# Performance work log

Measured on AMD Instinct MI355X. Metric: run time of the kernel, lower is better.

## Reference

```python
import jax, jax.numpy as jnp
import numpy as np
import math

H = 128  # hidden_dim
RADIUS = 30.0


def _lin(x, w, b):
    return x @ w + b


def _masked_softmax(logits, mask):
    return jax.nn.softmax(jnp.where(mask, logits, -1e9), axis=-1)


def setup_inputs() -> dict:
    key = jax.random.key(0)
    ks = iter(jax.random.split(key, 64))

    def p(shape, s=0.02):
        return (jax.random.normal(next(ks), shape, jnp.float32) * s)

    B, N, T, M, L = 2, 48, 24, 192, 20
    inp = {
        'agents_state': jax.random.normal(next(ks), (B, N, T, 5), jnp.float32),
        'agents_mask': jnp.ones((B, N, T), jnp.float32),
        'map_polylines': jax.random.normal(next(ks), (B, M, L, 2), jnp.float32),
        'map_poly_mask': jnp.ones((B, M), jnp.float32),
        'map_poly_type': jax.random.randint(next(ks), (B, M), 0, 4),
        'map_tl_status': jax.random.randint(next(ks), (B, M), 0, 8),
        'map_on_route': jax.random.randint(next(ks), (B, M), 0, 2),
        # AgentStateEncoder
        'ae_w0': p((5, H)), 'ae_b0': p((H,)), 'ae_w1': p((H, H)), 'ae_b1': p((H,)),
        'ae_w2': p((H, H)), 'ae_b2': p((H,)),
        # MapPolylineNodeEncoder point_mlp
        'mp_w0': p((2, H)), 'mp_b0': p((H,)), 'mp_w1': p((H, H)), 'mp_b1': p((H,)),
        'type_emb': p((4, H)), 'tl_emb': p((8, H)), 'route_emb': p((2, H)),
        'mo_w0': p((H, H)), 'mo_b0': p((H,)), 'mo_w1': p((H, H)), 'mo_b1': p((H,)),
        # map_rel_mlp (3 -> H -> 1)
        'mr_w0': p((3, H)), 'mr_b0': p((H,)), 'mr_w1': p((H, 1)), 'mr_b1': p((1,)),
        # nbr_rel_mlp (5 -> H -> 1)
        'nr_w0': p((5, H)), 'nr_b0': p((H,)), 'nr_w1': p((H, 1)), 'nr_b1': p((1,)),
        # tau_out (3H -> H -> 64)
        'to_w0': p((3 * H, H)), 'to_b0': p((H,)), 'to_w1': p((H, 64)), 'to_b1': p((64,)),
    }
    return inp


def reference(agents_state, agents_mask, map_polylines, map_poly_mask,
              map_poly_type, map_tl_status, map_on_route,
              ae_w0, ae_b0, ae_w1, ae_b1, ae_w2, ae_b2,
              mp_w0, mp_b0, mp_w1, mp_b1, type_emb, tl_emb, route_emb,
              mo_w0, mo_b0, mo_w1, mo_b1,
              mr_w0, mr_b0, mr_w1, mr_b1,
              nr_w0, nr_b0, nr_w1, nr_b1,
              to_w0, to_b0, to_w1, to_b1):
    B, N, T, _ = agents_state.shape
    a_mask = agents_mask > 0.5
    a_feat = agents_state[..., :5]

    # --- MapPolylineNodeEncoder ---
    m = map_poly_mask > 0.5
    h = jax.nn.relu(_lin(jax.nn.relu(_lin(map_polylines, mp_w0, mp_b0)), mp_w1, mp_b1))  # B,M,L,H
    h = h.max(axis=2)  # B,M,H
    pt = jnp.clip(map_poly_type, 0, type_emb.shape[0] - 1)
    tl = jnp.clip(map_tl_status, 0, tl_emb.shape[0] - 1)
    rt = jnp.clip(map_on_route, 0, route_emb.shape[0] - 1)
    h = h + type_emb[pt] + tl_emb[tl] + route_emb[rt]
    h = _lin(jax.nn.relu(_lin(h, mo_w0, mo_b0)), mo_w1, mo_b1)
    map_node = h * m[..., None].astype(h.dtype)  # B,M,D
    map_center = map_polylines.mean(axis=2)  # B,M,2

    # --- AgentStateEncoder ---
    a = jax.nn.relu(_lin(a_feat, ae_w0, ae_b0))
    a = jax.nn.relu(_lin(a, ae_w1, ae_b1))
    a_emb = _lin(a, ae_w2, ae_b2) * a_mask[..., None].astype(a.dtype)  # B,N,T,D

    # --- map cross-attention with relative-position bias ---
    agent_pos = a_feat[..., 0:2]
    rel = map_center[:, None, None, :, :] - agent_pos[:, :, :, None, :]  # B,N,T,M,2
    dist = jnp.linalg.norm(rel, axis=-1, keepdims=True)
    rel_feat = jnp.concatenate([rel, dist], axis=-1)  # B,N,T,M,3
    rel_score = _lin(jax.nn.relu(_lin(rel_feat, mr_w0, mr_b0)), mr_w1, mr_b1)[..., 0]  # B,N,T,M
    dot = jnp.einsum('bntd,bmd->bntm', a_emb, map_node) / math.sqrt(map_node.shape[-1])
    attn = _masked_softmax(dot + rel_score, m[:, None, None, :])
    map_ctx = jnp.einsum('bntm,bmd->bntd', attn, map_node)

    # --- neighbor graph attention ---
    pos = a_feat[..., 0:2]
    vel = a_feat[..., 3:5]
    rel_pos = jnp.transpose(pos[:, :, None] - pos[:, None, :], (0, 1, 3, 2, 4))  # B,N,T,N,2
    rel_vel = jnp.transpose(vel[:, :, None] - vel[:, None, :], (0, 1, 3, 2, 4))
    dist_ij = jnp.linalg.norm(rel_pos, axis=-1, keepdims=True)  # B,N,T,N,1
    rel_ij = jnp.concatenate([rel_pos, rel_vel, dist_ij], axis=-1)  # B,N,T,N,5
    nbr_score = _lin(jax.nn.relu(_lin(rel_ij, nr_w0, nr_b0)), nr_w1, nr_b1)[..., 0]  # B,N,T,N

    valid_i = a_mask[..., None]  # B,N,T,1
    valid_j = jnp.transpose(a_mask, (0, 2, 1))[:, None, :, :]  # B,1,T,N
    radius_ok = dist_ij[..., 0] <= RADIUS
    not_self = ~jnp.eye(N, dtype=bool)[None, :, None, :]  # 1,N,1,N
    nbr_mask = valid_i & valid_j & radius_ok & not_self

    dot_n = jnp.einsum('bntd,bjtd->bntj', a_emb, a_emb) / math.sqrt(a_emb.shape[-1])
    w_n = _masked_softmax(dot_n + nbr_score, nbr_mask)  # B,N,T,N
    nbr_ctx = jnp.einsum('bntj,bjtd->bntd', w_n, a_emb)

    tau = jnp.concatenate([a_emb, map_ctx, nbr_ctx], axis=-1)
    tau = _lin(jax.nn.relu(_lin(tau, to_w0, to_b0)), to_w1, to_b1)
    tau = tau * a_mask[..., None].astype(tau.dtype)
    return tau, map_ctx, nbr_ctx
```

## Files before the change

kernel.cpp:

```cpp
#include <hip/hip_runtime.h>
#include <math.h>

#define HH 128
#define BB 2
#define NN 48
#define TT 24
#define MM 192
#define LL 20
#define NT (BB*NN*TT)
#define RSQRT_H 0.08838834764831845f
#define RADIUS_C 30.0f

struct P {
    const float *astate, *amask, *polylines, *poly_mask;
    const int *ptype, *tlst, *route;
    const float *ae_w0,*ae_b0,*ae_w1,*ae_b1,*ae_w2,*ae_b2;
    const float *mp_w0,*mp_b0,*mp_w1,*mp_b1;
    const float *type_emb,*tl_emb,*route_emb;
    const float *mo_w0,*mo_b0,*mo_w1,*mo_b1;
    const float *mr_w0,*mr_b0,*mr_w1,*mr_b1;
    const float *nr_w0,*nr_b0,*nr_w1,*nr_b1;
    const float *to_w0,*to_b0,*to_w1,*to_b1;
    float *tau,*map_ctx,*nbr_ctx;
    float *a_emb,*map_node,*map_nodeT,*map_center;
};

struct SME { float pts[LL*2]; float h1T[HH][LL]; float mx[2][HH]; float hb[HH]; float pr[2][HH]; float hb2[HH]; };
struct SAG { float xin[2][5]; float h1[2][HH]; float h2[2][HH]; float p1[2][2][HH]; };

struct SF {
    float4 aq4L[HH];
    float  mctx[4][HH];
    float  nctx[4][HH];
    float  pc[2][4][HH];
    union {
        struct {
            float4 w4L[HH];
            float  w1L[HH];
            float  lg[4][MM];
            float4 p4L[MM];
            float  invL[4];
        } m;
        struct {
            float  pjL[NN][8];
            float4 wAL[HH];
            float4 wBL[HH];
            float  sPL[4][4][NN];
            float  dPL[4][4][NN];
            float  lgN[4][NN];
            float4 pN[NN];
        } n;
        struct {
            float4 xinT[3*HH];
            float4 h1T[HH];
        } t;
    } u;
};

__device__ void do_map_enc(const P& p, SME& s, int bm) {
    int tid = threadIdx.x, pp = tid >> 7, c = tid & 127;
    if (tid < LL*2) s.pts[tid] = p.polylines[(size_t)bm*LL*2 + tid];
    __syncthreads();
    {
        float w0x = p.mp_w0[c], w0y = p.mp_w0[HH + c], b0 = p.mp_b0[c];
        #pragma unroll
        for (int i = 0; i < 10; ++i) {
            int pt_ = pp*10 + i;
            s.h1T[c][pt_] = fmaxf(fmaf(s.pts[2*pt_], w0x, fmaf(s.pts[2*pt_+1], w0y, b0)), 0.f);
        }
    }
    if (tid < 2) {
        float sum = 0.f;
        for (int q = 0; q < LL; ++q) sum += s.pts[2*q + tid];
        p.map_center[bm*2 + tid] = sum * (1.0f / LL);
    }
    __syncthreads();
    {
        float acc[10];
        float b1 = p.mp_b1[c];
        #pragma unroll
        for (int i = 0; i < 10; ++i) acc[i] = b1;
        for (int k = 0; k < HH; ++k) {
            float wv = p.mp_w1[k*HH + c];
            const float* hrow = &s.h1T[k][pp*10];
            #pragma unroll
            for (int i = 0; i < 10; ++i) acc[i] = fmaf(hrow[i], wv, acc[i]);
        }
        float m10 = acc[0];
        #pragma unroll
        for (int i = 1; i < 10; ++i) m10 = fmaxf(m10, acc[i]);
        s.mx[pp][c] = m10;
    }
    __syncthreads();
    if (tid < HH) {
        float hm = fmaxf(fmaxf(s.mx[0][c], s.mx[1][c]), 0.f);
        int pt = p.ptype[bm]; pt = pt < 0 ? 0 : (pt > 3 ? 3 : pt);
        int tv = p.tlst[bm];  tv = tv < 0 ? 0 : (tv > 7 ? 7 : tv);
        int rv = p.route[bm]; rv = rv < 0 ? 0 : (rv > 1 ? 1 : rv);
        hm += p.type_emb[pt*HH + c] + p.tl_emb[tv*HH + c] + p.route_emb[rv*HH + c];
        s.hb[c] = hm;
    }
    __syncthreads();
    {
        float sum = 0.f;
        int k0 = pp*64;
        for (int k = k0; k < k0 + 64; ++k) sum = fmaf(s.hb[k], p.mo_w0[k*HH + c], sum);
        s.pr[pp][c] = sum;
    }
    __syncthreads();
    if (tid < HH) s.hb2[c] = fmaxf(s.pr[0][c] + s.pr[1][c] + p.mo_b0[c], 0.f);
    __syncthreads();
    {
        float sum = 0.f;
        int k0 = pp*64;
        for (int k = k0; k < k0 + 64; ++k) sum = fmaf(s.hb2[k], p.mo_w1[k*HH + c], sum);
        s.pr[pp][c] = sum;
    }
    __syncthreads();
    if (tid < HH) {
        float a3 = s.pr[0][c] + s.pr[1][c] + p.mo_b1[c];
        float mk = (p.poly_mask[bm] > 0.5f) ? 1.f : 0.f;
        float v = a3 * mk;
        p.map_node[(size_t)bm*HH + c] = v;
        int b = bm / MM, m = bm % MM;
        p.map_nodeT[((size_t)b*HH + c)*MM + m] = v;
    }
}

__device__ void do_agent_enc(const P& p, SAG& s, int r0) {
    int tid = threadIdx.x, h = tid >> 7, c = tid & 127;
    if (tid < 10) s.xin[tid/5][tid%5] = p.astate[(size_t)r0*5 + tid];
    __syncthreads();
    if (h == 0) {
        float b = p.ae_b0[c];
        float w[5];
        #pragma unroll
        for (int i = 0; i < 5; ++i) w[i] = p.ae_w0[i*HH + c];
        #pragma unroll
        for (int r = 0; r < 2; ++r) {
            float v = b;
            #pragma unroll
            for (int i = 0; i < 5; ++i) v = fmaf(s.xin[r][i], w[i], v);
            s.h1[r][c] = fmaxf(v, 0.f);
        }
    }
    __syncthreads();
    {
        float a0 = 0.f, a1 = 0.f;
        int k0 = h*64;
        for (int k = k0; k < k0 + 64; ++k) {
            float wv = p.ae_w1[k*HH + c];
            a0 = fmaf(s.h1[0][k], wv, a0);
            a1 = fmaf(s.h1[1][k], wv, a1);
        }
        s.p1[h][0][c] = a0; s.p1[h][1][c] = a1;
    }
    __syncthreads();
    {
        int r = h;
        s.h2[r][c] = fmaxf(s.p1[0][r][c] + s.p1[1][r][c] + p.ae_b1[c], 0.f);
    }
    __syncthreads();
    {
        float a0 = 0.f, a1 = 0.f;
        int k0 = h*64;
        for (int k = k0; k < k0 + 64; ++k) {
            float wv = p.ae_w2[k*HH + c];
            a0 = fmaf(s.h2[0][k], wv, a0);
            a1 = fmaf(s.h2[1][k], wv, a1);
        }
        s.p1[h][0][c] = a0; s.p1[h][1][c] = a1;
    }
    __syncthreads();
    {
        int r = h;
        int row = r0 + r;
        p.a_emb[(size_t)row*HH + c] = (s.p1[0][r][c] + s.p1[1][r][c] + p.ae_b2[c]) * p.amask[row];
    }
}

__global__ __launch_bounds__(256) void k_enc(P p) {
    __shared__ __align__(16) char smraw[(sizeof(SME) > sizeof(SAG)) ? sizeof(SME) : sizeof(SAG)];
    int task = blockIdx.x;
    if (task < BB*MM) do_map_enc(p, *(SME*)smraw, task);
    else              do_agent_enc(p, *(SAG*)smraw, (task - BB*MM)*2);
}

__global__ __launch_bounds__(256) void k_fat(P p) {
    __shared__ __align__(16) SF s;
    int task = blockIdx.x;
    int b    = task / (TT*12);
    int rem  = task % (TT*12);
    int t    = rem / 12;
    int n0   = (rem % 12) * 4;
    int tid  = threadIdx.x;

    int row0 = (b*NN + n0)*TT + t;

    for (int idx = tid; idx < 4*HH; idx += 256) {
        int r = idx >> 7, k = idx & 127;
        ((float*)&s.aq4L[k])[r] = p.a_emb[(size_t)(row0 + r*TT)*HH + k];
    }
    if (tid < HH) {
        int k = tid;
        s.u.m.w4L[k] = make_float4(p.mr_w0[k], p.mr_w0[HH+k], p.mr_w0[2*HH+k], p.mr_b0[k]);
        s.u.m.w1L[k] = p.mr_w1[k];
    }

    float rx[4], ry[4], rd[4];
    if (tid < MM) {
        float mcx = p.map_center[(b*MM + tid)*2];
        float mcy = p.map_center[(b*MM + tid)*2 + 1];
        #pragma unroll
        for (int r = 0; r < 4; ++r) {
            float px = p.astate[(size_t)(row0 + r*TT)*5];
            float py = p.astate[(size_t)(row0 + r*TT)*5 + 1];
            rx[r] = mcx - px; ry[r] = mcy - py;
            rd[r] = sqrtf(rx[r]*rx[r] + ry[r]*ry[r]);
        }
    }
    __syncthreads();

    if (tid < MM) {
        const float* mnc = p.map_nodeT + (size_t)b*HH*MM + tid;
        float sacc[4] = {0.f,0.f,0.f,0.f};
        float dt4[4]  = {0.f,0.f,0.f,0.f};
        const float4* w1q4 = (const float4*)s.u.m.w1L;
        for (int kq = 0; kq < HH/4; ++kq) {
            float4 w1q = w1q4[kq];
            #pragma unroll
            for (int j = 0; j < 4; ++j) {
                int k = kq*4 + j;
                float4 w  = s.u.m.w4L[k];
                float4 aq = s.aq4L[k];
                float  w1 = ((const float*)&w1q)[j];
                float  mn = mnc[(size_t)k*MM];
                #pragma unroll
                for (int r = 0; r < 4; ++r) {
                    float hv = fmaf(rx[r], w.x, fmaf(ry[r], w.y, fmaf(rd[r], w.z, w.w)));
                    sacc[r] = fmaf(fmaxf(hv, 0.f), w1, sacc[r]);
                }
                dt4[0] = fmaf(aq.x, mn, dt4[0]);
                dt4[1] = fmaf(aq.y, mn, dt4[1]);
                dt4[2] = fmaf(aq.z, mn, dt4[2]);
                dt4[3] = fmaf(aq.w, mn, dt4[3]);
            }
        }
        float pm = p.poly_mask[b*MM + tid];
        float b1 = p.mr_b1[0];
        #pragma unroll
        for (int r = 0; r < 4; ++r) {
            float lgt = fmaf(dt4[r], RSQRT_H, sacc[r] + b1);
            s.u.m.lg[r][tid] = (pm > 0.5f) ? lgt : -1e9f;
        }
    }
    __syncthreads();

    {
        int r = tid >> 6, l = tid & 63;
        float v = fmaxf(fmaxf(s.u.m.lg[r][l], s.u.m.lg[r][l+64]), s.u.m.lg[r][l+128]);
        #pragma unroll
        for (int o = 32; o > 0; o >>= 1) v = fmaxf(v, __shfl_xor(v, o));
        float e0 = expf(s.u.m.lg[r][l] - v);
        float e1 = expf(s.u.m.lg[r][l+64] - v);
        float e2 = expf(s.u.m.lg[r][l+128] - v);
        s.u.m.lg[r][l] = e0; s.u.m.lg[r][l+64] = e1; s.u.m.lg[r][l+128] = e2;
        float sm = e0 + e1 + e2;
        #pragma unroll
        for (int o = 32; o > 0; o >>= 1) sm += __shfl_xor(sm, o);
        if (l == 0) s.u.m.invL[r] = 1.0f / sm;
    }
    __syncthreads();
    if (tid < MM) {
        s.u.m.p4L[tid] = make_float4(s.u.m.lg[0][tid]*s.u.m.invL[0], s.u.m.lg[1][tid]*s.u.m.invL[1],
                                     s.u.m.lg[2][tid]*s.u.m.invL[2], s.u.m.lg[3][tid]*s.u.m.invL[3]);
    }
    __syncthreads();

    {
        int half = tid >> 7, c = tid & 127;
        float a0=0.f, a1=0.f, a2=0.f, a3=0.f;
        const float* mnb = p.map_node + ((size_t)b*MM + half*96)*HH + c;
        for (int m = 0; m < 96; ++m) {
            float mv = mnb[(size_t)m*HH];
            float4 pp4 = s.u.m.p4L[half*96 + m];
            a0 = fmaf(pp4.x, mv, a0); a1 = fmaf(pp4.y, mv, a1);
            a2 = fmaf(pp4.z, mv, a2); a3 = fmaf(pp4.w, mv, a3);
        }
        s.pc[half][0][c]=a0; s.pc[half][1][c]=a1; s.pc[half][2][c]=a2; s.pc[half][3][c]=a3;
    }
    __syncthreads();
    for (int idx = tid; idx < 4*HH; idx += 256) {
        int r = idx >> 7, c = idx & 127;
        float v = s.pc[0][r][c] + s.pc[1][r][c];
        s.mctx[r][c] = v;
        p.map_ctx[(size_t)(row0 + r*TT)*HH + c] = v;
    }
    __syncthreads();

    if (tid < NN) {
        int rj = (b*NN + tid)*TT + t;
        s.u.n.pjL[tid][0] = p.astate[(size_t)rj*5];
        s.u.n.pjL[tid][1] = p.astate[(size_t)rj*5 + 1];
        s.u.n.pjL[tid][2] = p.astate[(size_t)rj*5 + 3];
        s.u.n.pjL[tid][3] = p.astate[(size_t)rj*5 + 4];
        s.u.n.pjL[tid][4] = p.amask[rj];
    }
    if (tid < HH) {
        int k = tid;
        s.u.n.wAL[k] = make_float4(p.nr_w0[k], p.nr_w0[HH+k], p.nr_w0[2*HH+k], p.nr_w0[3*HH+k]);
        s.u.n.wBL[k] = make_float4(p.nr_w0[4*HH+k], p.nr_b0[k], p.nr_w1[k], 0.f);
    }
    __syncthreads();

    {
        int j  = tid % 48;
        int kg = tid / 48;
        if (kg < 4) {
            float jx = s.u.n.pjL[j][0], jy = s.u.n.pjL[j][1];
            float jvx = s.u.n.pjL[j][2], jvy = s.u.n.pjL[j][3];
            float dx[4], dy[4], dvx[4], dvy[4], dd[4];
            #pragma unroll
            for (int r = 0; r < 4; ++r) {
                int ni = n0 + r;
                dx[r]  = s.u.n.pjL[ni][0] - jx;  dy[r]  = s.u.n.pjL[ni][1] - jy;
                dvx[r] = s.u.n.pjL[ni][2] - jvx; dvy[r] = s.u.n.pjL[ni][3] - jvy;
                dd[r]  = sqrtf(dx[r]*dx[r] + dy[r]*dy[r]);
            }
            const float* aj = p.a_emb + ((size_t)(b*NN + j)*TT + t)*HH;
            float sr[4]  = {0.f,0.f,0.f,0.f};
            float dtn[4] = {0.f,0.f,0.f,0.f};
            int k0 = kg*32;
            #pragma unroll 4
            for (int kk = 0; kk < 32; ++kk) {
                int k = k0 + kk;
                float4 wa = s.u.n.wAL[k], wb = s.u.n.wBL[k];
                float4 aq = s.aq4L[k];
                float  av = aj[k];
                #pragma unroll
                for (int r = 0; r < 4; ++r) {
                    float hv = fmaf(dx[r], wa.x, fmaf(dy[r], wa.y,
                               fmaf(dvx[r], wa.z, fmaf(dvy[r], wa.w,
                               fmaf(dd[r], wb.x, wb.y)))));
                    sr[r] = fmaf(fmaxf(hv, 0.f), wb.z, sr[r]);
                }
                dtn[0] = fmaf(aq.x, av, dtn[0]); dtn[1] = fmaf(aq.y, av, dtn[1]);
                dtn[2] = fmaf(aq.z, av, dtn[2]); dtn[3] = fmaf(aq.w, av, dtn[3]);
            }
            #pragma unroll
            for (int r = 0; r < 4; ++r) { s.u.n.sPL[kg][r][j] = sr[r]; s.u.n.dPL[kg][r][j] = dtn[r]; }
        }
    }
    __syncthreads();

    {
        float b1 = p.nr_b1[0];
        for (int idx = tid; idx < 4*NN; idx += 256) {
            int r = idx / NN, jj = idx % NN;
            int ni = n0 + r;
            float ss  = s.u.n.sPL[0][r][jj] + s.u.n.sPL[1][r][jj] + s.u.n.sPL[2][r][jj] + s.u.n.sPL[3][r][jj] + b1;
            float do2 = s.u.n.dPL[0][r][jj] + s.u.n.dPL[1][r][jj] + s.u.n.dPL[2][r][jj] + s.u.n.dPL[3][r][jj];
            float ddx = s.u.n.pjL[ni][0] - s.u.n.pjL[jj][0];
            float ddy = s.u.n.pjL[ni][1] - s.u.n.pjL[jj][1];
            float dist = sqrtf(ddx*ddx + ddy*ddy);
            bool ok = (s.u.n.pjL[ni][4] > 0.5f) && (s.u.n.pjL[jj][4] > 0.5f) &&
                      (dist <= RADIUS_C) && (jj != ni);
            s.u.n.lgN[r][jj] = ok ? fmaf(do2, RSQRT_H, ss) : -1e9f;
        }
    }
    __syncthreads();

    {
        int r = tid >> 6, l = tid & 63;
        float v = (l < NN) ? s.u.n.lgN[r][l] : -3.4e38f;
        #pragma unroll
        for (int o = 32; o > 0; o >>= 1) v = fmaxf(v, __shfl_xor(v, o));
        float e = (l < NN) ? expf(s.u.n.lgN[r][l] - v) : 0.f;
        float sm = e;
        #pragma unroll
        for (int o = 32; o > 0; o >>= 1) sm += __shfl_xor(sm, o);
        if (l < NN) s.u.n.lgN[r][l] = e / sm;
    }
    __syncthreads();
    if (tid < NN) {
        s.u.n.pN[tid] = make_float4(s.u.n.lgN[0][tid], s.u.n.lgN[1][tid],
                                    s.u.n.lgN[2][tid], s.u.n.lgN[3][tid]);
    }
    __syncthreads();

    {
        int half = tid >> 7, c = tid & 127;
        float a0=0.f, a1=0.f, a2=0.f, a3=0.f;
        for (int jj = half*24; jj < half*24 + 24; ++jj) {
            float av = p.a_emb[((size_t)(b*NN + jj)*TT + t)*HH + c];
            float4 pp4 = s.u.n.pN[jj];
            a0 = fmaf(pp4.x, av, a0); a1 = fmaf(pp4.y, av, a1);
            a2 = fmaf(pp4.z, av, a2); a3 = fmaf(pp4.w, av, a3);
        }
        s.pc[half][0][c]=a0; s.pc[half][1][c]=a1; s.pc[half][2][c]=a2; s.pc[half][3][c]=a3;
    }
    __syncthreads();
    for (int idx = tid; idx < 4*HH; idx += 256) {
        int r = idx >> 7, c = idx & 127;
        float v = s.pc[0][r][c] + s.pc[1][r][c];
        s.nctx[r][c] = v;
        p.nbr_ctx[(size_t)(row0 + r*TT)*HH + c] = v;
    }
    __syncthreads();

    for (int idx = tid; idx < 3*HH; idx += 256) {
        if (idx < HH) {
            s.u.t.xinT[idx] = s.aq4L[idx];
        } else if (idx < 2*HH) {
            int k = idx - HH;
            s.u.t.xinT[idx] = make_float4(s.mctx[0][k], s.mctx[1][k], s.mctx[2][k], s.mctx[3][k]);
        } else {
            int k = idx - 2*HH;
            s.u.t.xinT[idx] = make_float4(s.nctx[0][k], s.nctx[1][k], s.nctx[2][k], s.nctx[3][k]);
        }
    }
    __syncthreads();
    {
        int c = tid & 127, h = tid >> 7;
        float acc[4] = {0,0,0,0};
        for (int k = h*192; k < h*192 + 192; ++k) {
            float wv = p.to_w0[k*HH + c];
            float4 x4 = s.u.t.xinT[k];
            acc[0]=fmaf(x4.x,wv,acc[0]); acc[1]=fmaf(x4.y,wv,acc[1]);
            acc[2]=fmaf(x4.z,wv,acc[2]); acc[3]=fmaf(x4.w,wv,acc[3]);
        }
        #pragma unroll
        for (int r = 0; r < 4; ++r) s.pc[h][r][c] = acc[r];
    }
    __syncthreads();
    for (int idx = tid; idx < 4*HH; idx += 256) {
        int r = idx >> 7, k = idx & 127;
        ((float*)&s.u.t.h1T[k])[r] = fmaxf(s.pc[0][r][k] + s.pc[1][r][k] + p.to_b0[k], 0.f);
    }
    __syncthreads();
    {
        int kh = tid >> 7, rc = tid & 127;
        int r = rc >> 6, c2 = rc & 63;
        float acc = 0.f;
        for (int k = kh*64; k < kh*64 + 64; ++k)
            acc = fmaf(((const float*)&s.u.t.h1T[k])[r], p.to_w1[k*64 + c2], acc);
        s.pc[kh][r][c2] = acc;
    }
    __syncthreads();
    if (tid < 128) {
        int r = tid >> 6, c2 = tid & 63;
        int row = row0 + r*TT;
        float v = (s.pc[0][r][c2] + s.pc[1][r][c2] + p.to_b1[c2]) * p.amask[row];
        p.tau[(size_t)row*64 + c2] = v;
    }
    __syncthreads();
    if (tid < 128) {
        int r = 2 + (tid >> 6), c2 = tid & 63;
        int row = row0 + r*TT;
        float acc = 0.f;
        for (int k = 0; k < HH; ++k)
            acc = fmaf(((const float*)&s.u.t.h1T[k])[r], p.to_w1[k*64 + c2], acc);
        float v = (acc + p.to_b1[c2]) * p.amask[row];
        p.tau[(size_t)row*64 + c2] = v;
    }
}

extern "C" void kernel_launch(void* const* d_in, const int* in_sizes, int n_in,
                              void* d_out, int out_size, void* d_ws, size_t ws_size,
                              hipStream_t stream)
{
    P p;
    p.astate    = (const float*)d_in[0];
    p.amask     = (const float*)d_in[1];
    p.polylines = (const float*)d_in[2];
    p.poly_mask = (const float*)d_in[3];
    p.ptype     = (const int*)d_in[4];
    p.tlst      = (const int*)d_in[5];
    p.route     = (const int*)d_in[6];
    p.ae_w0 = (const float*)d_in[7];  p.ae_b0 = (const float*)d_in[8];
    p.ae_w1 = (const float*)d_in[9];  p.ae_b1 = (const float*)d_in[10];
    p.ae_w2 = (const float*)d_in[11]; p.ae_b2 = (const float*)d_in[12];
    p.mp_w0 = (const float*)d_in[13]; p.mp_b0 = (const float*)d_in[14];
    p.mp_w1 = (const float*)d_in[15]; p.mp_b1 = (const float*)d_in[16];
    p.type_emb  = (const float*)d_in[17];
    p.tl_emb    = (const float*)d_in[18];
    p.route_emb = (const float*)d_in[19];
    p.mo_w0 = (const float*)d_in[20]; p.mo_b0 = (const float*)d_in[21];
    p.mo_w1 = (const float*)d_in[22]; p.mo_b1 = (const float*)d_in[23];
    p.mr_w0 = (const float*)d_in[24]; p.mr_b0 = (const float*)d_in[25];
    p.mr_w1 = (const float*)d_in[26]; p.mr_b1 = (const float*)d_in[27];
    p.nr_w0 = (const float*)d_in[28]; p.nr_b0 = (const float*)d_in[29];
    p.nr_w1 = (const float*)d_in[30]; p.nr_b1 = (const float*)d_in[31];
    p.to_w0 = (const float*)d_in[32]; p.to_b0 = (const float*)d_in[33];
    p.to_w1 = (const float*)d_in[34]; p.to_b1 = (const float*)d_in[35];

    p.tau     = (float*)d_out;
    p.map_ctx = (float*)d_out + (size_t)NT*64;
    p.nbr_ctx = p.map_ctx + (size_t)NT*HH;

    float* ws    = (float*)d_ws;
    p.a_emb      = ws;
    p.map_node   = p.a_emb + (size_t)NT*HH;
    p.map_nodeT  = p.map_node + (size_t)BB*MM*HH;
    p.map_center = p.map_nodeT + (size_t)BB*MM*HH;

    k_enc<<<BB*MM + NT/2, 256, 0, stream>>>(p);
    k_fat<<<BB*TT*12,     256, 0, stream>>>(p);
}
```

Baseline: 184.2 us.

## Double k_fat block size and split reductions across more thread groups

Raises k_fat to 512 threads and splits each reduction stage (map logits, map context, neighbor scores, neighbor context, both tau MLP layers) into more partial-sum groups, then combines them through shared memory. This adds parallelism within each of the 576 blocks, so per-thread serial loops get shorter and latency is easier to hide. It also changes the map encoder's h1 shared layout from transposed to row-major, which alters the LDS access pattern. In exchange it uses more shared memory and adds partial-sum buffers, which may lower occupancy.

```diff
diff --git a/kernel.cpp b/kernel.cpp
--- a/kernel.cpp
+++ b/kernel.cpp
@@ -25,18 +25,20 @@
     float *a_emb,*map_node,*map_nodeT,*map_center;
 };
 
-struct SME { float pts[LL*2]; float h1T[HH][LL]; float mx[2][HH]; float hb[HH]; float pr[2][HH]; float hb2[HH]; };
+struct SME { float pts[LL*2]; float h1[LL][HH]; float mx[2][HH]; float hb[HH]; float pr[2][HH]; float hb2[HH]; };
 struct SAG { float xin[2][5]; float h1[2][HH]; float h2[2][HH]; float p1[2][2][HH]; };
 
 struct SF {
     float4 aq4L[HH];
     float  mctx[4][HH];
     float  nctx[4][HH];
-    float  pc[2][4][HH];
+    float  pc[4][4][HH];
     union {
         struct {
             float4 w4L[HH];
             float  w1L[HH];
+            float4 pS[2][MM];
+            float4 pD[2][MM];
             float  lg[4][MM];
             float4 p4L[MM];
             float  invL[4];
@@ -45,8 +47,8 @@
             float  pjL[NN][8];
             float4 wAL[HH];
             float4 wBL[HH];
-            float  sPL[4][4][NN];
-            float  dPL[4][4][NN];
+            float  sPL[8][4][NN];
+            float  dPL[8][4][NN];
             float  lgN[4][NN];
             float4 pN[NN];
         } n;
@@ -65,8 +67,8 @@
         float w0x = p.mp_w0[c], w0y = p.mp_w0[HH + c], b0 = p.mp_b0[c];
         #pragma unroll
         for (int i = 0; i < 10; ++i) {
-            int pt_ = pp*10 + i;
-            s.h1T[c][pt_] = fmaxf(fmaf(s.pts[2*pt_], w0x, fmaf(s.pts[2*pt_+1], w0y, b0)), 0.f);
+            int pt_ = pp + 2*i;
+            s.h1[pt_][c] = fmaxf(fmaf(s.pts[2*pt_], w0x, fmaf(s.pts[2*pt_+1], w0y, b0)), 0.f);
         }
     }
     if (tid < 2) {
@@ -82,9 +84,8 @@
         for (int i = 0; i < 10; ++i) acc[i] = b1;
         for (int k = 0; k < HH; ++k) {
             float wv = p.mp_w1[k*HH + c];
-            const float* hrow = &s.h1T[k][pp*10];
             #pragma unroll
-            for (int i = 0; i < 10; ++i) acc[i] = fmaf(hrow[i], wv, acc[i]);
+            for (int i = 0; i < 10; ++i) acc[i] = fmaf(s.h1[pp + 2*i][k], wv, acc[i]);
         }
         float m10 = acc[0];
         #pragma unroll
@@ -186,7 +187,7 @@
     else              do_agent_enc(p, *(SAG*)smraw, (task - BB*MM)*2);
 }
 
-__global__ __launch_bounds__(256) void k_fat(P p) {
+__global__ __launch_bounds__(512) void k_fat(P p) {
     __shared__ __align__(16) SF s;
     int task = blockIdx.x;
     int b    = task / (TT*12);
@@ -197,8 +198,8 @@
 
     int row0 = (b*NN + n0)*TT + t;
 
-    for (int idx = tid; idx < 4*HH; idx += 256) {
-        int r = idx >> 7, k = idx & 127;
+    {
+        int r = tid >> 7, k = tid & 127;
         ((float*)&s.aq4L[k])[r] = p.a_emb[(size_t)(row0 + r*TT)*HH + k];
     }
     if (tid < HH) {
@@ -207,10 +208,12 @@
         s.u.m.w1L[k] = p.mr_w1[k];
     }
 
+    int g  = tid >> 8;
+    int ml = tid & 255;
     float rx[4], ry[4], rd[4];
-    if (tid < MM) {
-        float mcx = p.map_center[(b*MM + tid)*2];
-        float mcy = p.map_center[(b*MM + tid)*2 + 1];
+    if (ml < MM) {
+        float mcx = p.map_center[(b*MM + ml)*2];
+        float mcy = p.map_center[(b*MM + ml)*2 + 1];
         #pragma unroll
         for (int r = 0; r < 4; ++r) {
             float px = p.astate[(size_t)(row0 + r*TT)*5];
@@ -221,42 +224,50 @@
     }
     __syncthreads();
 
-    if (tid < MM) {
-        const float* mnc = p.map_nodeT + (size_t)b*HH*MM + tid;
+    if (ml < MM) {
+        const float* mnc = p.map_nodeT + (size_t)b*HH*MM + ml;
         float sacc[4] = {0.f,0.f,0.f,0.f};
         float dt4[4]  = {0.f,0.f,0.f,0.f};
-        const float4* w1q4 = (const float4*)s.u.m.w1L;
-        for (int kq = 0; kq < HH/4; ++kq) {
-            float4 w1q = w1q4[kq];
+        int k0 = g*64;
+        #pragma unroll 4
+        for (int kk = 0; kk < 64; ++kk) {
+            int k = k0 + kk;
+            float4 w  = s.u.m.w4L[k];
+            float4 aq = s.aq4L[k];
+            float  w1 = s.u.m.w1L[k];
+            float  mn = mnc[(size_t)k*MM];
             #pragma unroll
-            for (int j = 0; j < 4; ++j) {
-                int k = kq*4 + j;
-                float4 w  = s.u.m.w4L[k];
-                float4 aq = s.aq4L[k];
-                float  w1 = ((const float*)&w1q)[j];
-                float  mn = mnc[(size_t)k*MM];
-                #pragma unroll
-                for (int r = 0; r < 4; ++r) {
-                    float hv = fmaf(rx[r], w.x, fmaf(ry[r], w.y, fmaf(rd[r], w.z, w.w)));
-                    sacc[r] = fmaf(fmaxf(hv, 0.f), w1, sacc[r]);
-                }
-                dt4[0] = fmaf(aq.x, mn, dt4[0]);
-                dt4[1] = fmaf(aq.y, mn, dt4[1]);
-                dt4[2] = fmaf(aq.z, mn, dt4[2]);
-                dt4[3] = fmaf(aq.w, mn, dt4[3]);
+            for (int r = 0; r < 4; ++r) {
+                float hv = fmaf(rx[r], w.x, fmaf(ry[r], w.y, fmaf(rd[r], w.z, w.w)));
+                sacc[r] = fmaf(fmaxf(hv, 0.f), w1, sacc[r]);
             }
-        }
+            dt4[0] = fmaf(aq.x, mn, dt4[0]);
+            dt4[1] = fmaf(aq.y, mn, dt4[1]);
+            dt4[2] = fmaf(aq.z, mn, dt4[2]);
+            dt4[3] = fmaf(aq.w, mn, dt4[3]);
+        }
+        s.u.m.pS[g][ml] = make_float4(sacc[0], sacc[1], sacc[2], sacc[3]);
+        s.u.m.pD[g][ml] = make_float4(dt4[0],  dt4[1],  dt4[2],  dt4[3]);
+    }
+    __syncthreads();
+    if (tid < MM) {
+        float4 sA = s.u.m.pS[0][tid], sB = s.u.m.pS[1][tid];
+        float4 dA = s.u.m.pD[0][tid], dB = s.u.m.pD[1][tid];
         float pm = p.poly_mask[b*MM + tid];
         float b1 = p.mr_b1[0];
-        #pragma unroll
-        for (int r = 0; r < 4; ++r) {
-            float lgt = fmaf(dt4[r], RSQRT_H, sacc[r] + b1);
-            s.u.m.lg[r][tid] = (pm > 0.5f) ? lgt : -1e9f;
-        }
-    }
-    __syncthreads();
-
-    {
+        float lg0 = fmaf(dA.x + dB.x, RSQRT_H, sA.x + sB.x + b1);
+        float lg1 = fmaf(dA.y + dB.y, RSQRT_H, sA.y + sB.y + b1);
+        float lg2 = fmaf(dA.z + dB.z, RSQRT_H, sA.z + sB.z + b1);
+        float lg3 = fmaf(dA.w + dB.w, RSQRT_H, sA.w + sB.w + b1);
+        bool ok = pm > 0.5f;
+        s.u.m.lg[0][tid] = ok ? lg0 : -1e9f;
+        s.u.m.lg[1][tid] = ok ? lg1 : -1e9f;
+        s.u.m.lg[2][tid] = ok ? lg2 : -1e9f;
+        s.u.m.lg[3][tid] = ok ? lg3 : -1e9f;
+    }
+    __syncthreads();
+
+    if (tid < 256) {
         int r = tid >> 6, l = tid & 63;
         float v = fmaxf(fmaxf(s.u.m.lg[r][l], s.u.m.lg[r][l+64]), s.u.m.lg[r][l+128]);
         #pragma unroll
@@ -278,21 +289,21 @@
     __syncthreads();
 
     {
-        int half = tid >> 7, c = tid & 127;
+        int gq = tid >> 7, c = tid & 127;
         float a0=0.f, a1=0.f, a2=0.f, a3=0.f;
-        const float* mnb = p.map_node + ((size_t)b*MM + half*96)*HH + c;
-        for (int m = 0; m < 96; ++m) {
+        const float* mnb = p.map_node + ((size_t)b*MM + gq*48)*HH + c;
+        for (int m = 0; m < 48; ++m) {
             float mv = mnb[(size_t)m*HH];
-            float4 pp4 = s.u.m.p4L[half*96 + m];
+            float4 pp4 = s.u.m.p4L[gq*48 + m];
             a0 = fmaf(pp4.x, mv, a0); a1 = fmaf(pp4.y, mv, a1);
             a2 = fmaf(pp4.z, mv, a2); a3 = fmaf(pp4.w, mv, a3);
         }
-        s.pc[half][0][c]=a0; s.pc[half][1][c]=a1; s.pc[half][2][c]=a2; s.pc[half][3][c]=a3;
-    }
-    __syncthreads();
-    for (int idx = tid; idx < 4*HH; idx += 256) {
-        int r = idx >> 7, c = idx & 127;
-        float v = s.pc[0][r][c] + s.pc[1][r][c];
+        s.pc[gq][0][c]=a0; s.pc[gq][1][c]=a1; s.pc[gq][2][c]=a2; s.pc[gq][3][c]=a3;
+    }
+    __syncthreads();
+    {
+        int r = tid >> 7, c = tid & 127;
+        float v = s.pc[0][r][c] + s.pc[1][r][c] + s.pc[2][r][c] + s.pc[3][r][c];
         s.mctx[r][c] = v;
         p.map_ctx[(size_t)(row0 + r*TT)*HH + c] = v;
     }
@@ -316,7 +327,7 @@
     {
         int j  = tid % 48;
         int kg = tid / 48;
-        if (kg < 4) {
+        if (kg < 8) {
             float jx = s.u.n.pjL[j][0], jy = s.u.n.pjL[j][1];
             float jvx = s.u.n.pjL[j][2], jvy = s.u.n.pjL[j][3];
             float dx[4], dy[4], dvx[4], dvy[4], dd[4];
@@ -330,9 +341,9 @@
             const float* aj = p.a_emb + ((size_t)(b*NN + j)*TT + t)*HH;
             float sr[4]  = {0.f,0.f,0.f,0.f};
             float dtn[4] = {0.f,0.f,0.f,0.f};
-            int k0 = kg*32;
+            int k0 = kg*16;
             #pragma unroll 4
-            for (int kk = 0; kk < 32; ++kk) {
+            for (int kk = 0; kk < 16; ++kk) {
                 int k = k0 + kk;
                 float4 wa = s.u.n.wAL[k], wb = s.u.n.wBL[k];
                 float4 aq = s.aq4L[k];
@@ -353,24 +364,23 @@
     }
     __syncthreads();
 
-    {
+    if (tid < 4*NN) {
+        int r = tid / NN, jj = tid % NN;
+        int ni = n0 + r;
         float b1 = p.nr_b1[0];
-        for (int idx = tid; idx < 4*NN; idx += 256) {
-            int r = idx / NN, jj = idx % NN;
-            int ni = n0 + r;
-            float ss  = s.u.n.sPL[0][r][jj] + s.u.n.sPL[1][r][jj] + s.u.n.sPL[2][r][jj] + s.u.n.sPL[3][r][jj] + b1;
-            float do2 = s.u.n.dPL[0][r][jj] + s.u.n.dPL[1][r][jj] + s.u.n.dPL[2][r][jj] + s.u.n.dPL[3][r][jj];
-            float ddx = s.u.n.pjL[ni][0] - s.u.n.pjL[jj][0];
-            float ddy = s.u.n.pjL[ni][1] - s.u.n.pjL[jj][1];
-            float dist = sqrtf(ddx*ddx + ddy*ddy);
-            bool ok = (s.u.n.pjL[ni][4] > 0.5f) && (s.u.n.pjL[jj][4] > 0.5f) &&
-                      (dist <= RADIUS_C) && (jj != ni);
-            s.u.n.lgN[r][jj] = ok ? fmaf(do2, RSQRT_H, ss) : -1e9f;
-        }
-    }
-    __syncthreads();
-
-    {
+        float ss = b1, do2 = 0.f;
+        #pragma unroll
+        for (int q = 0; q < 8; ++q) { ss += s.u.n.sPL[q][r][jj]; do2 += s.u.n.dPL[q][r][jj]; }
+        float ddx = s.u.n.pjL[ni][0] - s.u.n.pjL[jj][0];
+        float ddy = s.u.n.pjL[ni][1] - s.u.n.pjL[jj][1];
+        float dist = sqrtf(ddx*ddx + ddy*ddy);
+        bool ok = (s.u.n.pjL[ni][4] > 0.5f) && (s.u.n.pjL[jj][4] > 0.5f) &&
+                  (dist <= RADIUS_C) && (jj != ni);
+        s.u.n.lgN[r][jj] = ok ? fmaf(do2, RSQRT_H, ss) : -1e9f;
+    }
+    __syncthreads();
+
+    if (tid < 256) {
         int r = tid >> 6, l = tid & 63;
         float v = (l < NN) ? s.u.n.lgN[r][l] : -3.4e38f;
         #pragma unroll
@@ -389,26 +399,27 @@
     __syncthreads();
 
     {
-        int half = tid >> 7, c = tid & 127;
+        int gq = tid >> 7, c = tid & 127;
         float a0=0.f, a1=0.f, a2=0.f, a3=0.f;
-        for (int jj = half*24; jj < half*24 + 24; ++jj) {
+        for (int jj = gq*12; jj < gq*12 + 12; ++jj) {
             float av = p.a_emb[((size_t)(b*NN + jj)*TT + t)*HH + c];
             float4 pp4 = s.u.n.pN[jj];
             a0 = fmaf(pp4.x, av, a0); a1 = fmaf(pp4.y, av, a1);
             a2 = fmaf(pp4.z, av, a2); a3 = fmaf(pp4.w, av, a3);
         }
-        s.pc[half][0][c]=a0; s.pc[half][1][c]=a1; s.pc[half][2][c]=a2; s.pc[half][3][c]=a3;
-    }
-    __syncthreads();
-    for (int idx = tid; idx < 4*HH; idx += 256) {
-        int r = idx >> 7, c = idx & 127;
-        float v = s.pc[0][r][c] + s.pc[1][r][c];
+        s.pc[gq][0][c]=a0; s.pc[gq][1][c]=a1; s.pc[gq][2][c]=a2; s.pc[gq][3][c]=a3;
+    }
+    __syncthreads();
+    {
+        int r = tid >> 7, c = tid & 127;
+        float v = s.pc[0][r][c] + s.pc[1][r][c] + s.pc[2][r][c] + s.pc[3][r][c];
         s.nctx[r][c] = v;
         p.nbr_ctx[(size_t)(row0 + r*TT)*HH + c] = v;
     }
     __syncthreads();
 
-    for (int idx = tid; idx < 3*HH; idx += 256) {
+    if (tid < 3*HH) {
+        int idx = tid;
         if (idx < HH) {
             s.u.t.xinT[idx] = s.aq4L[idx];
         } else if (idx < 2*HH) {
@@ -421,9 +432,9 @@
     }
     __syncthreads();
     {
-        int c = tid & 127, h = tid >> 7;
+        int h = tid >> 7, c = tid & 127;
         float acc[4] = {0,0,0,0};
-        for (int k = h*192; k < h*192 + 192; ++k) {
+        for (int k = h*96; k < h*96 + 96; ++k) {
             float wv = p.to_w0[k*HH + c];
             float4 x4 = s.u.t.xinT[k];
             acc[0]=fmaf(x4.x,wv,acc[0]); acc[1]=fmaf(x4.y,wv,acc[1]);
@@ -433,13 +444,14 @@
         for (int r = 0; r < 4; ++r) s.pc[h][r][c] = acc[r];
     }
     __syncthreads();
-    for (int idx = tid; idx < 4*HH; idx += 256) {
-        int r = idx >> 7, k = idx & 127;
-        ((float*)&s.u.t.h1T[k])[r] = fmaxf(s.pc[0][r][k] + s.pc[1][r][k] + p.to_b0[k], 0.f);
-    }
-    __syncthreads();
-    {
-        int kh = tid >> 7, rc = tid & 127;
+    {
+        int r = tid >> 7, k = tid & 127;
+        float v = s.pc[0][r][k] + s.pc[1][r][k] + s.pc[2][r][k] + s.pc[3][r][k] + p.to_b0[k];
+        ((float*)&s.u.t.h1T[k])[r] = fmaxf(v, 0.f);
+    }
+    __syncthreads();
+    {
+        int kh = tid >> 8, rc = tid & 255;
         int r = rc >> 6, c2 = rc & 63;
         float acc = 0.f;
         for (int k = kh*64; k < kh*64 + 64; ++k)
@@ -447,20 +459,10 @@
         s.pc[kh][r][c2] = acc;
     }
     __syncthreads();
-    if (tid < 128) {
+    if (tid < 256) {
         int r = tid >> 6, c2 = tid & 63;
         int row = row0 + r*TT;
         float v = (s.pc[0][r][c2] + s.pc[1][r][c2] + p.to_b1[c2]) * p.amask[row];
-        p.tau[(size_t)row*64 + c2] = v;
-    }
-    __syncthreads();
-    if (tid < 128) {
-        int r = 2 + (tid >> 6), c2 = tid & 63;
-        int row = row0 + r*TT;
-        float acc = 0.f;
-        for (int k = 0; k < HH; ++k)
-            acc = fmaf(((const float*)&s.u.t.h1T[k])[r], p.to_w1[k*64 + c2], acc);
-        float v = (acc + p.to_b1[c2]) * p.amask[row];
         p.tau[(size_t)row*64 + c2] = v;
     }
 }
@@ -505,5 +507,5 @@
     p.map_center = p.map_nodeT + (size_t)BB*MM*HH;
 
     k_enc<<<BB*MM + NT/2, 256, 0, stream>>>(p);
-    k_fat<<<BB*TT*12,     256, 0, stream>>>(p);
+    k_fat<<<BB*TT*12,     512, 0, stream>>>(p);
 }
```

Measured after the change: 184.6 us. About the same (+0.2%).
